# Kernel optimization log

Measured on AMD Instinct MI355X. Metric: run time of the kernel, lower is better.

Reference implementation:

```python
import jax, jax.numpy as jnp
import numpy as np

B, N, L, D = 1, 128, 256, 256   # batch, num_seqs, seq_len, msa_dim
P, H = 128, 8                   # pair_dim, num_heads
DH = D // H                     # head_dim


def setup_inputs() -> dict:
    key = jax.random.key(0)
    ks = jax.random.split(key, 7)
    msa = jax.random.normal(ks[0], (B, N, L, D), dtype=jnp.float32)
    pair = jax.random.normal(ks[1], (B, L, L, P), dtype=jnp.float32)
    mask = jax.random.randint(ks[2], (B, N, L), 0, 2) > 0  # bool key mask
    w_qkv = jax.random.normal(ks[3], (D, 3 * D), dtype=jnp.float32) * (D ** -0.5)
    w_pb = jax.random.normal(ks[4], (P, H), dtype=jnp.float32) * (P ** -0.5)
    b_pb = jnp.zeros((H,), dtype=jnp.float32)
    w_out = jax.random.normal(ks[5], (D, D), dtype=jnp.float32) * (D ** -0.5)
    b_out = jnp.zeros((D,), dtype=jnp.float32)
    return {"msa": msa, "pair": pair, "mask": mask, "w_qkv": w_qkv,
            "w_pb": w_pb, "b_pb": b_pb, "w_out": w_out, "b_out": b_out}


def reference(msa, pair, mask, w_qkv, w_pb, b_pb, w_out, b_out):
    b, n, l, d = msa.shape
    scaling = DH ** -0.5
    qkv = msa @ w_qkv                                   # [b,n,l,3d]
    qkv = qkv.reshape(b, n, l, 3, H, DH)
    q, k, v = qkv[..., 0, :, :], qkv[..., 1, :, :], qkv[..., 2, :, :]  # [b,n,l,h,dh]
    pair_bias = (pair @ w_pb + b_pb)                    # [b,l,l,h]
    pair_bias = jnp.transpose(pair_bias, (0, 3, 1, 2))  # [b,h,l,l]
    # scores: [b,n,h,l,l]
    dots = jnp.einsum('bnqhd,bnkhd->bnhqk', q, k) * scaling
    dots = dots + pair_bias[:, None]                    # broadcast over num_seqs
    dots = jnp.where(mask[:, :, None, None, :], dots, -jnp.inf)  # mask keys
    attn = jax.nn.softmax(dots, axis=-1)
    out = jnp.einsum('bnhqk,bnkhd->bnqhd', attn, v)     # [b,n,l,h,dh]
    out = out.reshape(b, n, l, d)
    return out @ w_out + b_out
```

## Files before the change

### kernel.cpp

```cpp
#include <hip/hip_runtime.h>
#include <hip/hip_bf16.h>

#define NN 128
#define LL 256
#define DD 256
#define PP 128
#define HH 8
#define DHH 32

typedef __bf16 bf16x8 __attribute__((ext_vector_type(8)));
typedef float f32x4 __attribute__((ext_vector_type(4)));

__global__ __launch_bounds__(256) void cvt_bf16(
    const float* __restrict__ src, __hip_bfloat16* __restrict__ dst, int n) {
  for (int i = (blockIdx.x * 256 + threadIdx.x) * 4; i < n; i += gridDim.x * 1024) {
    float4 v = *(const float4*)(src + i);
    ushort4 o;
    o.x = __bfloat16_as_ushort(__float2bfloat16(v.x));
    o.y = __bfloat16_as_ushort(__float2bfloat16(v.y));
    o.z = __bfloat16_as_ushort(__float2bfloat16(v.z));
    o.w = __bfloat16_as_ushort(__float2bfloat16(v.w));
    *(ushort4*)(dst + i) = o;
  }
}

__global__ __launch_bounds__(256) void transpose_cvt(
    const float* __restrict__ src, __hip_bfloat16* __restrict__ dst,
    int K, int N) {
  __shared__ float t[32][33];
  int n0 = blockIdx.x * 32, k0 = blockIdx.y * 32;
  int tx = threadIdx.x & 31, ty = threadIdx.x >> 5;
  for (int i = 0; i < 4; ++i) {
    int ky = ty + i * 8;
    t[ky][tx] = src[(size_t)(k0 + ky) * N + n0 + tx];
  }
  __syncthreads();
  for (int i = 0; i < 4; ++i) {
    int ny = ty + i * 8;
    dst[(size_t)(n0 + ny) * K + k0 + tx] = __float2bfloat16(t[tx][ny]);
  }
}

__global__ __launch_bounds__(256) void bias_transpose(
    const float* __restrict__ src, float* __restrict__ dst) {
  __shared__ float t[32][33];
  int h = blockIdx.z;
  int q0 = blockIdx.y * 32, k0 = blockIdx.x * 32;
  int tx = threadIdx.x & 31, ty = threadIdx.x >> 5;
  const float* s = src + (size_t)h * LL * LL;
  float* d = dst + (size_t)h * LL * LL;
  for (int i = 0; i < 4; ++i) {
    int qy = ty + i * 8;
    t[qy][tx] = s[(size_t)(q0 + qy) * LL + k0 + tx];
  }
  __syncthreads();
  for (int i = 0; i < 4; ++i) {
    int ky = ty + i * 8;
    d[(size_t)(k0 + ky) * LL + q0 + tx] = t[tx][ky] - 12.0f;
  }
}

#define MODE_I32 0
#define MODE_I8 1
#define MODE_BF16 2
#define MODE_F32 3

__global__ __launch_bounds__(256) void mask_expand(
    const unsigned char* __restrict__ mraw, int* __restrict__ mout) {
  __shared__ int s_or1, s_or2, s_or3, s_max, s_mode;
  int tid = threadIdx.x;
  if (tid == 0) { s_or1 = 0; s_or2 = 0; s_or3 = 0; s_max = 0; }
  __syncthreads();
  int or1 = 0, or2 = 0, or3 = 0, mx = 0;
  for (int j = tid; j < 4096; j += 256) {
    int b = mraw[j];
    mx = mx > b ? mx : b;
    int r = j & 3;
    if (r == 1) or1 |= b;
    else if (r == 2) or2 |= b;
    else if (r == 3) or3 |= b;
  }
  atomicOr(&s_or1, or1); atomicOr(&s_or2, or2); atomicOr(&s_or3, or3);
  atomicMax(&s_max, mx);
  __syncthreads();
  if (tid == 0) {
    int mode;
    if (s_max <= 1) mode = ((s_or1 | s_or2 | s_or3) == 0) ? MODE_I32 : MODE_I8;
    else            mode = (s_or1 != 0) ? MODE_BF16 : MODE_F32;
    s_mode = mode;
  }
  __syncthreads();
  int mode = s_mode;
  int i0 = blockIdx.x * 1024;
  for (int i = i0 + tid; i < i0 + 1024; i += 256) {
    int v;
    if (mode == MODE_I32)       v = ((const int*)mraw)[i] != 0;
    else if (mode == MODE_I8)   v = mraw[i] != 0;
    else if (mode == MODE_BF16) v = ((const unsigned short*)mraw)[i] != 0;
    else                        v = ((const unsigned int*)mraw)[i] != 0;
    mout[i] = v;
  }
}

#define GEMM_MAINLOOP(Aptr, Btptr)                                            \
  __shared__ __align__(16) __hip_bfloat16 Asm[128 * 32];                      \
  __shared__ __align__(16) __hip_bfloat16 Bsm[128 * 32];                      \
  int tid = threadIdx.x;                                                      \
  int lane = tid & 63;                                                        \
  int wv = tid >> 6;                                                          \
  int wm = (wv >> 1) * 64, wn = (wv & 1) * 64;                                \
  int lr = lane & 15, quad = lane >> 4;                                       \
  int bm = blockIdx.x, bn = blockIdx.y;                                       \
  f32x4 acc[4][4];                                                            \
  for (int i = 0; i < 4; ++i)                                                 \
    for (int j = 0; j < 4; ++j) acc[i][j] = (f32x4){0.f, 0.f, 0.f, 0.f};      \
  for (int ks = 0; ks < 8; ++ks) {                                            \
    int k0 = ks * 32;                                                         \
    if (ks) __syncthreads();                                                  \
    for (int i = 0; i < 2; ++i) {                                             \
      int c = tid + i * 256;                                                  \
      int row = c >> 2, cc = c & 3;                                           \
      ((uint4*)Asm)[c] =                                                      \
          *(const uint4*)(Aptr + ((size_t)(bm * 128 + row)) * 256 + k0 + cc * 8); \
      ((uint4*)Bsm)[c] =                                                      \
          *(const uint4*)(Btptr + ((size_t)(bn * 128 + row)) * 256 + k0 + cc * 8); \
    }                                                                         \
    __syncthreads();                                                          \
    bf16x8 af[4], bfr[4];                                                     \
    for (int mi = 0; mi < 4; ++mi)                                            \
      af[mi] = *(const bf16x8*)&Asm[(wm + mi * 16 + lr) * 32 + quad * 8];     \
    for (int ni = 0; ni < 4; ++ni)                                            \
      bfr[ni] = *(const bf16x8*)&Bsm[(wn + ni * 16 + lr) * 32 + quad * 8];    \
    for (int mi = 0; mi < 4; ++mi)                                            \
      for (int ni = 0; ni < 4; ++ni)                                          \
        acc[mi][ni] = __builtin_amdgcn_mfma_f32_16x16x32_bf16(                \
            af[mi], bfr[ni], acc[mi][ni], 0, 0, 0);                           \
  }

__global__ __launch_bounds__(256) void qkv_gemm_mfma(
    const __hip_bfloat16* __restrict__ A,
    const __hip_bfloat16* __restrict__ Bt,
    __hip_bfloat16* __restrict__ qb,
    __hip_bfloat16* __restrict__ kb,
    __hip_bfloat16* __restrict__ vb) {
  GEMM_MAINLOOP(A, Bt)
  for (int mi = 0; mi < 4; ++mi) {
    for (int ni = 0; ni < 4; ++ni) {
      int gcol = bn * 128 + wn + ni * 16 + lr;
      int t = gcol >> 8, rem = gcol & 255;
      int h = rem >> 5, dh = rem & 31;
      for (int r = 0; r < 4; ++r) {
        int grow = bm * 128 + wm + mi * 16 + quad * 4 + r;
        int n = grow >> 8, l = grow & 255;
        __hip_bfloat16 val = __float2bfloat16(acc[mi][ni][r]);
        if (t == 0)
          qb[(size_t)(((n * HH + h) * LL + l)) * DHH + dh] = val;
        else if (t == 1)
          kb[(size_t)(((n * HH + h) * LL + l)) * DHH + dh] = val;
        else
          vb[(size_t)(((n * HH + h) * DHH + dh)) * LL + l] = val;
      }
    }
  }
}

__global__ __launch_bounds__(256) void out_gemm_mfma(
    const __hip_bfloat16* __restrict__ A,
    const __hip_bfloat16* __restrict__ Bt,
    const float* __restrict__ bout,
    float* __restrict__ C) {
  GEMM_MAINLOOP(A, Bt)
  for (int mi = 0; mi < 4; ++mi) {
    for (int ni = 0; ni < 4; ++ni) {
      int gcol = bn * 128 + wn + ni * 16 + lr;
      float bo = bout[gcol];
      for (int r = 0; r < 4; ++r) {
        int grow = bm * 128 + wm + mi * 16 + quad * 4 + r;
        C[(size_t)grow * 256 + gcol] = acc[mi][ni][r] + bo;
      }
    }
  }
}

__global__ __launch_bounds__(256) void pair_bias_kernel(
    const float* __restrict__ pair,
    const float* __restrict__ w_pb,
    const float* __restrict__ b_pb,
    float* __restrict__ bias) {
  __shared__ float wp[128][9];
  __shared__ float rows[32][129];
  int tid = threadIdx.x;
  for (int i = 0; i < 4; ++i) {
    int e = tid + i * 256;
    wp[e >> 3][e & 7] = w_pb[e];
  }
  int row0 = blockIdx.x * 32;
  const float* src = pair + (size_t)row0 * PP;
  for (int i = 0; i < 16; ++i) {
    int e = tid + i * 256;
    int r = e >> 7, c = e & 127;
    rows[r][c] = src[r * 128 + c];
  }
  __syncthreads();
  int h = tid >> 5, rl = tid & 31;
  float acc = b_pb[h];
  for (int p = 0; p < 128; ++p)
    acc += rows[rl][p] * wp[p][h];
  int row = row0 + rl;
  int i = row >> 8, j = row & 255;
  bias[((size_t)(h * LL + i)) * LL + j] = acc;
}

__global__ __launch_bounds__(256) void attn_mfma(
    const __hip_bfloat16* __restrict__ qb,
    const __hip_bfloat16* __restrict__ kb,
    const __hip_bfloat16* __restrict__ vbt,
    const float* __restrict__ biasTs,
    const int* __restrict__ mask,
    __hip_bfloat16* __restrict__ ao) {
  __shared__ __align__(16) __hip_bfloat16 Psm[4][16][68];
  int bx = blockIdx.x;
  int h = bx >> 7, n = bx & 127;
  int nh = n * HH + h;
  int tid = threadIdx.x, lane = tid & 63, wv = tid >> 6;
  int lr = lane & 15, quad = lane >> 4;
  int wm = wv * 64;
  size_t base = (size_t)nh * (LL * DHH);

  const __hip_bfloat16* qp = qb + base;
  const __hip_bfloat16* kp = kb + base;
  const __hip_bfloat16* vp = vbt + base;
  const float* bT = biasTs + (size_t)h * LL * LL;

  unsigned mkb = 0;
  const int* mrow = mask + n * LL;
  for (int kt = 0; kt < 4; ++kt)
    for (int nj = 0; nj < 4; ++nj)
      if (mrow[kt * 64 + nj * 16 + lr]) mkb |= 1u << (kt * 4 + nj);

  bf16x8 aq[4];
  for (int mi = 0; mi < 4; ++mi)
    aq[mi] = *(const bf16x8*)(qp + (size_t)(wm + mi * 16 + lr) * DHH + quad * 8);

  const float scale = 0.17677669529663687f;

  float lsum[4][4];
  f32x4 o_acc[4][2];
  for (int mi = 0; mi < 4; ++mi)
    for (int r = 0; r < 4; ++r) lsum[mi][r] = 0.f;
  for (int mi = 0; mi < 4; ++mi)
    for (int no = 0; no < 2; ++no) o_acc[mi][no] = (f32x4){0.f, 0.f, 0.f, 0.f};

  for (int kt = 0; kt < 4; ++kt) {
    int j0 = kt * 64;
    bf16x8 bk[4];
    for (int nj = 0; nj < 4; ++nj)
      bk[nj] = *(const bf16x8*)(kp + (size_t)(j0 + nj * 16 + lr) * DHH + quad * 8);
    bf16x8 bv[2][2];
    for (int ks = 0; ks < 2; ++ks)
      for (int no = 0; no < 2; ++no)
        bv[ks][no] = *(const bf16x8*)(vp + (size_t)(no * 16 + lr) * LL +
                                      j0 + ks * 32 + quad * 8);

    f32x4 s[4][4];
    for (int mi = 0; mi < 4; ++mi)
      for (int nj = 0; nj < 4; ++nj) s[mi][nj] = (f32x4){0.f, 0.f, 0.f, 0.f};
    for (int mi = 0; mi < 4; ++mi)
      for (int nj = 0; nj < 4; ++nj)
        s[mi][nj] = __builtin_amdgcn_mfma_f32_16x16x32_bf16(
            aq[mi], bk[nj], s[mi][nj], 0, 0, 0);

    for (int nj = 0; nj < 4; ++nj) {
      int col = j0 + nj * 16 + lr;
      bool mk = (mkb >> (kt * 4 + nj)) & 1u;
      const float* bcol = bT + (size_t)col * LL;
      for (int mi = 0; mi < 4; ++mi) {
        f32x4 b4 = *(const f32x4*)(bcol + wm + mi * 16 + quad * 4);
        for (int r = 0; r < 4; ++r) {
          float p = __expf(fmaf(s[mi][nj][r], scale, b4[r]));
          p = mk ? p : 0.f;
          s[mi][nj][r] = p;
          lsum[mi][r] += p;
        }
      }
    }

    for (int mi = 0; mi < 4; ++mi) {
      for (int nj = 0; nj < 4; ++nj)
        for (int r = 0; r < 4; ++r)
          Psm[wv][quad * 4 + r][nj * 16 + lr] = __float2bfloat16(s[mi][nj][r]);
      for (int ks = 0; ks < 2; ++ks) {
        bf16x8 ap = *(const bf16x8*)&Psm[wv][lr][ks * 32 + quad * 8];
        for (int no = 0; no < 2; ++no)
          o_acc[mi][no] = __builtin_amdgcn_mfma_f32_16x16x32_bf16(
              ap, bv[ks][no], o_acc[mi][no], 0, 0, 0);
      }
    }
  }

  for (int mi = 0; mi < 4; ++mi)
    for (int r = 0; r < 4; ++r) {
      float ls = lsum[mi][r];
      for (int off = 1; off < 16; off <<= 1) ls += __shfl_xor(ls, off);
      float inv = (ls > 0.f) ? 1.f / ls : 0.f;
      int l_idx = wm + mi * 16 + quad * 4 + r;
      for (int no = 0; no < 2; ++no) {
        int dh = no * 16 + lr;
        ao[(((size_t)n * LL + l_idx) * HH + h) * DHH + dh] =
            __float2bfloat16(o_acc[mi][no][r] * inv);
      }
    }
}

extern "C" void kernel_launch(void* const* d_in, const int* in_sizes, int n_in,
                              void* d_out, int out_size, void* d_ws, size_t ws_size,
                              hipStream_t stream) {
  const float* msa   = (const float*)d_in[0];
  const float* pair  = (const float*)d_in[1];
  const unsigned char* mask = (const unsigned char*)d_in[2];
  const float* w_qkv = (const float*)d_in[3];
  const float* w_pb  = (const float*)d_in[4];
  const float* b_pb  = (const float*)d_in[5];
  const float* w_out = (const float*)d_in[6];
  const float* b_out = (const float*)d_in[7];
  float* out = (float*)d_out;

  char* ws = (char*)d_ws;
  __hip_bfloat16* qb      = (__hip_bfloat16*)(ws);
  __hip_bfloat16* kb      = (__hip_bfloat16*)(ws + 16777216);
  __hip_bfloat16* vb      = (__hip_bfloat16*)(ws + 33554432);
  __hip_bfloat16* msa_c   = (__hip_bfloat16*)(ws + 50331648);
  __hip_bfloat16* ao      = (__hip_bfloat16*)(ws + 50331648);
  float*          bias    = (float*)(ws + 67108864);
  float*          biasT   = (float*)(ws + 69206016);
  __hip_bfloat16* wqkv_t  = (__hip_bfloat16*)(ws + 71303168);
  __hip_bfloat16* wout_t  = (__hip_bfloat16*)(ws + 71696384);
  int*            msk     = (int*)(ws + 71827456);

  mask_expand<<<32, 256, 0, stream>>>(mask, msk);
  cvt_bf16<<<1024, 256, 0, stream>>>(msa, msa_c, NN * LL * DD);
  transpose_cvt<<<dim3(24, 8), 256, 0, stream>>>(w_qkv, wqkv_t, 256, 768);
  transpose_cvt<<<dim3(8, 8), 256, 0, stream>>>(w_out, wout_t, 256, 256);

  qkv_gemm_mfma<<<dim3(256, 6), 256, 0, stream>>>(msa_c, wqkv_t, qb, kb, vb);
  pair_bias_kernel<<<2048, 256, 0, stream>>>(pair, w_pb, b_pb, bias);
  bias_transpose<<<dim3(8, 8, 8), 256, 0, stream>>>(bias, biasT);
  attn_mfma<<<1024, 256, 0, stream>>>(qb, kb, vb, biasT, msk, ao);
  out_gemm_mfma<<<dim3(256, 2), 256, 0, stream>>>(ao, wout_t, b_out, out);
}
```

Before: 256.1 us.

## Swap MFMA operand order to keep P in registers and drop bias transpose

The QK^T MFMA now runs with operands swapped so each lane holds a key-column strip of scores. That strip feeds the 16x16x16 PV MFMA directly as the B operand, which removes the LDS round-trip for P. Because the scores are now laid out with the query as row, the bias is read in its original [h,q,k] layout, so the separate bias_transpose kernel goes away and the -12 shift moves into pair_bias_kernel. The mask becomes a per-element multiply, and the output writes are vectorised. The trade-off is more, smaller MFMAs (16x16x16 instead of 16x16x32) and per-lane mask loads.

```diff
diff --git a/kernel.cpp b/kernel.cpp
--- a/kernel.cpp
+++ b/kernel.cpp
@@ -9,7 +9,9 @@
 #define DHH 32
 
 typedef __bf16 bf16x8 __attribute__((ext_vector_type(8)));
+typedef short s16x4 __attribute__((ext_vector_type(4)));
 typedef float f32x4 __attribute__((ext_vector_type(4)));
+typedef unsigned int u32x2 __attribute__((ext_vector_type(2)));
 
 __global__ __launch_bounds__(256) void cvt_bf16(
     const float* __restrict__ src, __hip_bfloat16* __restrict__ dst, int n) {
@@ -38,25 +40,6 @@
   for (int i = 0; i < 4; ++i) {
     int ny = ty + i * 8;
     dst[(size_t)(n0 + ny) * K + k0 + tx] = __float2bfloat16(t[tx][ny]);
-  }
-}
-
-__global__ __launch_bounds__(256) void bias_transpose(
-    const float* __restrict__ src, float* __restrict__ dst) {
-  __shared__ float t[32][33];
-  int h = blockIdx.z;
-  int q0 = blockIdx.y * 32, k0 = blockIdx.x * 32;
-  int tx = threadIdx.x & 31, ty = threadIdx.x >> 5;
-  const float* s = src + (size_t)h * LL * LL;
-  float* d = dst + (size_t)h * LL * LL;
-  for (int i = 0; i < 4; ++i) {
-    int qy = ty + i * 8;
-    t[qy][tx] = s[(size_t)(q0 + qy) * LL + k0 + tx];
-  }
-  __syncthreads();
-  for (int i = 0; i < 4; ++i) {
-    int ky = ty + i * 8;
-    d[(size_t)(k0 + ky) * LL + q0 + tx] = t[tx][ky] - 12.0f;
   }
 }
 
@@ -203,7 +186,7 @@
   }
   __syncthreads();
   int h = tid >> 5, rl = tid & 31;
-  float acc = b_pb[h];
+  float acc = b_pb[h] - 12.0f;
   for (int p = 0; p < 128; ++p)
     acc += rows[rl][p] * wp[p][h];
   int row = row0 + rl;
@@ -215,10 +198,9 @@
     const __hip_bfloat16* __restrict__ qb,
     const __hip_bfloat16* __restrict__ kb,
     const __hip_bfloat16* __restrict__ vbt,
-    const float* __restrict__ biasTs,
+    const float* __restrict__ biasQ,
     const int* __restrict__ mask,
     __hip_bfloat16* __restrict__ ao) {
-  __shared__ __align__(16) __hip_bfloat16 Psm[4][16][68];
   int bx = blockIdx.x;
   int h = bx >> 7, n = bx & 127;
   int nh = n * HH + h;
@@ -230,86 +212,97 @@
   const __hip_bfloat16* qp = qb + base;
   const __hip_bfloat16* kp = kb + base;
   const __hip_bfloat16* vp = vbt + base;
-  const float* bT = biasTs + (size_t)h * LL * LL;
-
-  unsigned mkb = 0;
+  const float* bQ = biasQ + (size_t)h * LL * LL;
   const int* mrow = mask + n * LL;
-  for (int kt = 0; kt < 4; ++kt)
-    for (int nj = 0; nj < 4; ++nj)
-      if (mrow[kt * 64 + nj * 16 + lr]) mkb |= 1u << (kt * 4 + nj);
+
+  const float scale = 0.17677669529663687f;
 
   bf16x8 aq[4];
+#pragma unroll
   for (int mi = 0; mi < 4; ++mi)
     aq[mi] = *(const bf16x8*)(qp + (size_t)(wm + mi * 16 + lr) * DHH + quad * 8);
 
-  const float scale = 0.17677669529663687f;
-
-  float lsum[4][4];
+  float lsum[4] = {0.f, 0.f, 0.f, 0.f};
   f32x4 o_acc[4][2];
+#pragma unroll
   for (int mi = 0; mi < 4; ++mi)
-    for (int r = 0; r < 4; ++r) lsum[mi][r] = 0.f;
-  for (int mi = 0; mi < 4; ++mi)
+#pragma unroll
     for (int no = 0; no < 2; ++no) o_acc[mi][no] = (f32x4){0.f, 0.f, 0.f, 0.f};
 
+#pragma unroll
   for (int kt = 0; kt < 4; ++kt) {
     int j0 = kt * 64;
     bf16x8 bk[4];
+#pragma unroll
     for (int nj = 0; nj < 4; ++nj)
       bk[nj] = *(const bf16x8*)(kp + (size_t)(j0 + nj * 16 + lr) * DHH + quad * 8);
-    bf16x8 bv[2][2];
-    for (int ks = 0; ks < 2; ++ks)
+    s16x4 av[4][2];
+#pragma unroll
+    for (int nj = 0; nj < 4; ++nj)
+#pragma unroll
       for (int no = 0; no < 2; ++no)
-        bv[ks][no] = *(const bf16x8*)(vp + (size_t)(no * 16 + lr) * LL +
-                                      j0 + ks * 32 + quad * 8);
-
-    f32x4 s[4][4];
-    for (int mi = 0; mi < 4; ++mi)
-      for (int nj = 0; nj < 4; ++nj) s[mi][nj] = (f32x4){0.f, 0.f, 0.f, 0.f};
-    for (int mi = 0; mi < 4; ++mi)
+        av[nj][no] = *(const s16x4*)(vp + (size_t)(no * 16 + lr) * LL +
+                                     j0 + nj * 16 + quad * 4);
+    f32x4 mw[4];
+#pragma unroll
+    for (int nj = 0; nj < 4; ++nj) {
+      int4 m4 = *(const int4*)(mrow + j0 + nj * 16 + quad * 4);
+      mw[nj][0] = m4.x ? 1.f : 0.f;
+      mw[nj][1] = m4.y ? 1.f : 0.f;
+      mw[nj][2] = m4.z ? 1.f : 0.f;
+      mw[nj][3] = m4.w ? 1.f : 0.f;
+    }
+
+#pragma unroll
+    for (int mi = 0; mi < 4; ++mi) {
+      f32x4 s[4];
+#pragma unroll
       for (int nj = 0; nj < 4; ++nj)
-        s[mi][nj] = __builtin_amdgcn_mfma_f32_16x16x32_bf16(
-            aq[mi], bk[nj], s[mi][nj], 0, 0, 0);
-
-    for (int nj = 0; nj < 4; ++nj) {
-      int col = j0 + nj * 16 + lr;
-      bool mk = (mkb >> (kt * 4 + nj)) & 1u;
-      const float* bcol = bT + (size_t)col * LL;
-      for (int mi = 0; mi < 4; ++mi) {
-        f32x4 b4 = *(const f32x4*)(bcol + wm + mi * 16 + quad * 4);
-        for (int r = 0; r < 4; ++r) {
-          float p = __expf(fmaf(s[mi][nj][r], scale, b4[r]));
-          p = mk ? p : 0.f;
-          s[mi][nj][r] = p;
-          lsum[mi][r] += p;
-        }
+        s[nj] = __builtin_amdgcn_mfma_f32_16x16x32_bf16(
+            bk[nj], aq[mi], (f32x4){0.f, 0.f, 0.f, 0.f}, 0, 0, 0);
+
+      const float* brow = bQ + (size_t)(wm + mi * 16 + lr) * LL + j0;
+#pragma unroll
+      for (int nj = 0; nj < 4; ++nj) {
+        f32x4 b4 = *(const f32x4*)(brow + nj * 16 + quad * 4);
+        float p0 = __expf(fmaf(s[nj][0], scale, b4[0])) * mw[nj][0];
+        float p1 = __expf(fmaf(s[nj][1], scale, b4[1])) * mw[nj][1];
+        float p2 = __expf(fmaf(s[nj][2], scale, b4[2])) * mw[nj][2];
+        float p3 = __expf(fmaf(s[nj][3], scale, b4[3])) * mw[nj][3];
+        lsum[mi] += (p0 + p1) + (p2 + p3);
+        unsigned lo = ((unsigned)__bfloat16_as_ushort(__float2bfloat16(p1)) << 16) |
+                      (unsigned)__bfloat16_as_ushort(__float2bfloat16(p0));
+        unsigned hi = ((unsigned)__bfloat16_as_ushort(__float2bfloat16(p3)) << 16) |
+                      (unsigned)__bfloat16_as_ushort(__float2bfloat16(p2));
+        u32x2 pu = {lo, hi};
+        s16x4 pb = __builtin_bit_cast(s16x4, pu);
+#pragma unroll
+        for (int no = 0; no < 2; ++no)
+          o_acc[mi][no] = __builtin_amdgcn_mfma_f32_16x16x16bf16_1k(
+              av[nj][no], pb, o_acc[mi][no], 0, 0, 0);
       }
     }
-
-    for (int mi = 0; mi < 4; ++mi) {
-      for (int nj = 0; nj < 4; ++nj)
-        for (int r = 0; r < 4; ++r)
-          Psm[wv][quad * 4 + r][nj * 16 + lr] = __float2bfloat16(s[mi][nj][r]);
-      for (int ks = 0; ks < 2; ++ks) {
-        bf16x8 ap = *(const bf16x8*)&Psm[wv][lr][ks * 32 + quad * 8];
-        for (int no = 0; no < 2; ++no)
-          o_acc[mi][no] = __builtin_amdgcn_mfma_f32_16x16x32_bf16(
-              ap, bv[ks][no], o_acc[mi][no], 0, 0, 0);
-      }
-    }
-  }
-
-  for (int mi = 0; mi < 4; ++mi)
-    for (int r = 0; r < 4; ++r) {
-      float ls = lsum[mi][r];
-      for (int off = 1; off < 16; off <<= 1) ls += __shfl_xor(ls, off);
-      float inv = (ls > 0.f) ? 1.f / ls : 0.f;
-      int l_idx = wm + mi * 16 + quad * 4 + r;
-      for (int no = 0; no < 2; ++no) {
-        int dh = no * 16 + lr;
-        ao[(((size_t)n * LL + l_idx) * HH + h) * DHH + dh] =
-            __float2bfloat16(o_acc[mi][no][r] * inv);
-      }
-    }
+  }
+
+#pragma unroll
+  for (int mi = 0; mi < 4; ++mi) {
+    float ls = lsum[mi];
+    ls += __shfl_xor(ls, 16);
+    ls += __shfl_xor(ls, 32);
+    float inv = (ls > 0.f) ? 1.f / ls : 0.f;
+    int q = wm + mi * 16 + lr;
+#pragma unroll
+    for (int no = 0; no < 2; ++no) {
+      f32x4 o = o_acc[mi][no];
+      ushort4 w;
+      w.x = __bfloat16_as_ushort(__float2bfloat16(o[0] * inv));
+      w.y = __bfloat16_as_ushort(__float2bfloat16(o[1] * inv));
+      w.z = __bfloat16_as_ushort(__float2bfloat16(o[2] * inv));
+      w.w = __bfloat16_as_ushort(__float2bfloat16(o[3] * inv));
+      *(ushort4*)(ao + (size_t)n * (LL * DD) + (size_t)q * DD +
+                  h * DHH + no * 16 + quad * 4) = w;
+    }
+  }
 }
 
 extern "C" void kernel_launch(void* const* d_in, const int* in_sizes, int n_in,
@@ -332,7 +325,6 @@
   __hip_bfloat16* msa_c   = (__hip_bfloat16*)(ws + 50331648);
   __hip_bfloat16* ao      = (__hip_bfloat16*)(ws + 50331648);
   float*          bias    = (float*)(ws + 67108864);
-  float*          biasT   = (float*)(ws + 69206016);
   __hip_bfloat16* wqkv_t  = (__hip_bfloat16*)(ws + 71303168);
   __hip_bfloat16* wout_t  = (__hip_bfloat16*)(ws + 71696384);
   int*            msk     = (int*)(ws + 71827456);
@@ -344,7 +336,6 @@
 
   qkv_gemm_mfma<<<dim3(256, 6), 256, 0, stream>>>(msa_c, wqkv_t, qb, kb, vb);
   pair_bias_kernel<<<2048, 256, 0, stream>>>(pair, w_pb, b_pb, bias);
-  bias_transpose<<<dim3(8, 8, 8), 256, 0, stream>>>(bias, biasT);
-  attn_mfma<<<1024, 256, 0, stream>>>(qb, kb, vb, biasT, msk, ao);
+  attn_mfma<<<1024, 256, 0, stream>>>(qb, kb, vb, bias, msk, ao);
   out_gemm_mfma<<<dim3(256, 2), 256, 0, stream>>>(ao, wout_t, b_out, out);
 }
```

New measurement: 256.9 us. No clear change (+0.3%).
